# Optimization experiments

Hardware: AMD Instinct MI355X
Metric: run time of the kernel (lower is better)

## Reference

```python
import jax, jax.numpy as jnp
import numpy as np

B, N, D = 8, 2048, 128

def setup_inputs() -> dict:
    key = jax.random.key(0)
    k1, k2, k3 = jax.random.split(key, 3)
    h = jax.random.normal(k1, (B, N, D), dtype=jnp.float32)
    W = jax.random.normal(k2, (D, D), dtype=jnp.float32) * (1.0 / np.sqrt(D))
    # a has shape [1,1,1,2D] in torch; flatten to [2D] (xavier-normal init)
    a = jax.random.normal(k3, (2 * D,), dtype=jnp.float32) * np.sqrt(2.0 / (2 * D))
    return {"h": h, "W": W, "a": a}

def reference(h, W, a):
    act = jax.nn.relu
    # h <- h @ W^T (nn.Linear with weight W means x @ W.T; here W is the weight matrix)
    hw = jnp.einsum('bnd,ed->bne', h, W)  # [B,N,D]
    a_i, a_j = a[:D], a[D:]
    # e_ij = act(a_i . h_i + a_j . h_j) -- equivalent to sum(cat(h_i,h_j)*a, -1)
    s_i = jnp.einsum('bnd,d->bn', hw, a_i)  # [B,N]
    s_j = jnp.einsum('bnd,d->bn', hw, a_j)  # [B,N]
    e = act(s_i[:, :, None] + s_j[:, None, :])  # [B,N,N]
    a_ij = jax.nn.softmax(e, axis=2)
    out = act(jnp.einsum('bij,bjd->bid', a_ij, hw))
    return out
```

## Files before the change

### kernel.cpp

```cpp
#include <hip/hip_runtime.h>
#include <hip/hip_bf16.h>

#define BB 8
#define NN 2048
#define DD 128
#define TI 32
#define HP 132
#define CH 32
#define NC (NN / CH)
#define NO (NC + 1)
#define NFIX (BB * NO)

__device__ __forceinline__ float relu(float x) { return x > 0.f ? x : 0.f; }

__global__ __launch_bounds__(256) void GraphAttentionalLayer_1168231104632_kernel(
    const float* __restrict__ h,
    const float* __restrict__ W,
    const float* __restrict__ a,
    float* __restrict__ hw,
    float* __restrict__ E,
    float* __restrict__ F)
{
    __shared__ float h_s[TI][HP];
    __shared__ float wt_s[32][HP];

    const int tid = threadIdx.x;
    const int t = tid & 127;
    const int hh = tid >> 7;
    const int tx = tid & 31, ty = tid >> 5;
    const int b = blockIdx.x >> 6;
    const int i0 = (blockIdx.x & 63) * TI;
    const size_t base = ((size_t)b * NN + i0) * DD;

    for (int r = hh; r < TI; r += 2)
        h_s[r][t] = h[base + (size_t)r * DD + t];

    const int e0 = tx * 4, r0 = ty * 4;
    float acc[4][4];
#pragma unroll
    for (int i = 0; i < 4; i++)
#pragma unroll
        for (int j = 0; j < 4; j++) acc[i][j] = 0.f;

    for (int dc = 0; dc < DD; dc += 32) {
        __syncthreads();
#pragma unroll
        for (int q = 0; q < 16; q++) {
            const int g = q * 256 + tid;
            const int e = g >> 5;
            const int d2 = g & 31;
            wt_s[d2][e] = W[(size_t)e * DD + dc + d2];
        }
        __syncthreads();
#pragma unroll 4
        for (int dd = 0; dd < 32; dd++) {
            const float4 wv = *reinterpret_cast<const float4*>(&wt_s[dd][e0]);
            const float w4[4] = {wv.x, wv.y, wv.z, wv.w};
#pragma unroll
            for (int r = 0; r < 4; r++) {
                const float hv = h_s[r0 + r][dc + dd];
#pragma unroll
                for (int e = 0; e < 4; e++) acc[r][e] += hv * w4[e];
            }
        }
    }

#pragma unroll
    for (int r = 0; r < 4; r++) {
        float4 o = make_float4(acc[r][0], acc[r][1], acc[r][2], acc[r][3]);
        *reinterpret_cast<float4*>(&hw[base + (size_t)(r0 + r) * DD + e0]) = o;
    }

    const float4 aiv = *reinterpret_cast<const float4*>(&a[e0]);
    const float4 ajv = *reinterpret_cast<const float4*>(&a[DD + e0]);
    const float ai4[4] = {aiv.x, aiv.y, aiv.z, aiv.w};
    const float aj4[4] = {ajv.x, ajv.y, ajv.z, ajv.w};
#pragma unroll
    for (int r = 0; r < 4; r++) {
        float pi = 0.f, pj = 0.f;
#pragma unroll
        for (int e = 0; e < 4; e++) { pi += acc[r][e] * ai4[e]; pj += acc[r][e] * aj4[e]; }
#pragma unroll
        for (int off = 16; off > 0; off >>= 1) {
            pi += __shfl_down(pi, off, 32);
            pj += __shfl_down(pj, off, 32);
        }
        if (tx == 0) {
            const size_t row = (size_t)b * NN + i0 + r0 + r;
            E[row] = __expf(pi);
            F[row] = __expf(pj);
        }
    }
}

__global__ __launch_bounds__(256) void GraphAttentionalLayer_1168231104632_rank(
    const float* __restrict__ F,
    float* __restrict__ Fsorted,
    int* __restrict__ perm)
{
    __shared__ float F_s[NN];
    __shared__ int   part[4][64];

    const int t = threadIdx.x;
    const int b = blockIdx.x >> 5;
    const int j0 = (blockIdx.x & 31) * 64;
    const size_t nb = (size_t)b * NN;

    for (int q = 0; q < NN / 256; q++)
        F_s[q * 256 + t] = F[nb + q * 256 + t];
    __syncthreads();

    const int tj = t & 63, ts = t >> 6;
    const int j = j0 + tj;
    const float fj = F_s[j];
    const int m0 = ts * (NN / 4);
    int cnt = 0;
#pragma unroll 8
    for (int mi = 0; mi < NN / 4; mi++) {
        const int m = m0 + mi;
        const float fm = F_s[m];
        cnt += (fm < fj) | ((fm == fj) & (m < j));
    }
    part[ts][tj] = cnt;
    __syncthreads();
    if (ts == 0) {
        const int r = part[0][tj] + part[1][tj] + part[2][tj] + part[3][tj];
        Fsorted[nb + r] = fj;
        perm[nb + r] = j;
    }
}

__global__ __launch_bounds__(128) void GraphAttentionalLayer_1168231104632_scan(
    const float* __restrict__ hw,
    const float* __restrict__ Fsorted,
    const int* __restrict__ perm,
    float* __restrict__ Q0L, float* __restrict__ Q1L,
    float* __restrict__ C0,  float* __restrict__ C1)
{
    const int t = threadIdx.x;
    const int b = blockIdx.x / NC, c = blockIdx.x % NC;
    const size_t nb = (size_t)b * NN;
    const int m0 = c * CH;

    int   jv[CH];
    float Fv[CH];
#pragma unroll
    for (int mm = 0; mm < CH; mm++) jv[mm] = perm[nb + m0 + mm];
#pragma unroll
    for (int mm = 0; mm < CH; mm++) Fv[mm] = Fsorted[nb + m0 + mm];

    float hv[CH];
#pragma unroll
    for (int mm = 0; mm < CH; mm++)
        hv[mm] = hw[(nb + jv[mm]) * DD + t];

    float a0 = 0.f, a1 = 0.f;
#pragma unroll
    for (int mm = 0; mm < CH; mm++) {
        const int m = m0 + mm;
        Q0L[(nb + m) * DD + t] = a0;
        Q1L[(nb + m) * DD + t] = a1;
        a0 += hv[mm];
        a1 += Fv[mm] * hv[mm];
    }
    C0[((size_t)b * NC + c) * DD + t] = a0;
    C1[((size_t)b * NC + c) * DD + t] = a1;
}

__global__ __launch_bounds__(256) void GraphAttentionalLayer_1168231104632_mid(
    const float* __restrict__ C0, const float* __restrict__ C1,
    const float* __restrict__ Fsorted, const float* __restrict__ E,
    float* __restrict__ O0, float* __restrict__ O1,
    int* __restrict__ kk,  float* __restrict__ zinv)
{
    __shared__ float fs_s[NN];
    __shared__ float cf_s[NC];
    __shared__ float of_s[NO];

    const int tid = threadIdx.x;

    if (blockIdx.x < NFIX) {
        const int b = blockIdx.x / NO, c = blockIdx.x % NO;
        const int d = tid & 127;
        const float* C = (tid < 128) ? C0 : C1;
        float*       O = (tid < 128) ? O0 : O1;
        float o = 0.f;
        int c2 = 0;
        for (; c2 + 16 <= c; c2 += 16) {
            float v[16];
#pragma unroll
            for (int q = 0; q < 16; q++)
                v[q] = C[((size_t)b * NC + c2 + q) * DD + d];
#pragma unroll
            for (int q = 0; q < 16; q++) o += v[q];
        }
        for (; c2 < c; c2++)
            o += C[((size_t)b * NC + c2) * DD + d];
        O[((size_t)b * NO + c) * DD + d] = o;
        return;
    }

    const int sb = blockIdx.x - NFIX;
    const int b = sb >> 3;
    const int i0 = (sb & 7) * 256;
    const size_t nb = (size_t)b * NN;

    for (int q = 0; q < NN / 256; q++)
        fs_s[q * 256 + tid] = Fsorted[nb + q * 256 + tid];
    __syncthreads();

    if (tid < NC) {
        float p = 0.f;
        const int m0 = tid * CH;
#pragma unroll
        for (int mm = 0; mm < CH; mm++) p += fs_s[m0 + mm];
        cf_s[tid] = p;
    }
    __syncthreads();
    if (tid < NO) {
        float p = 0.f;
        for (int c2 = 0; c2 < tid; c2++) p += cf_s[c2];
        of_s[tid] = p;
    }
    __syncthreads();

    const int row = (int)nb + i0 + tid;
    const float Ei = E[row];
    const float thr = 1.0f / Ei;
    int lo = 0, hi = NN;
    while (lo < hi) {
        const int mid = (lo + hi) >> 1;
        if (fs_s[mid] < thr) lo = mid + 1; else hi = mid;
    }
    float fpl = 0.f;
    for (int m = (lo >> 5) << 5; m < lo; m++) fpl += fs_s[m];
    const float TF = of_s[NC];
    const float Pk = of_s[lo >> 5] + fpl;
    const float z = Ei * (TF - Pk) + (float)lo;
    kk[row] = lo;
    zinv[row] = 1.0f / z;
}

__global__ __launch_bounds__(128) void GraphAttentionalLayer_1168231104632_out(
    const float* __restrict__ Q0L, const float* __restrict__ Q1L,
    const float* __restrict__ O0,  const float* __restrict__ O1,
    const int* __restrict__ kk,    const float* __restrict__ zinv,
    const float* __restrict__ E,   float* __restrict__ out)
{
    const int t = threadIdx.x;
    const int row = blockIdx.x;
    const int b = row >> 11;
    const size_t nb = (size_t)b * NN;

    const int k = kk[row];
    const float Ev = E[row];
    const float zv = zinv[row];
    const float T1 = O1[((size_t)b * NO + NC) * DD + t];

    float num;
    if (k < NN) {
        const int c = k >> 5;
        const float q0 = Q0L[(nb + k) * DD + t] + O0[((size_t)b * NO + c) * DD + t];
        const float q1 = Q1L[(nb + k) * DD + t] + O1[((size_t)b * NO + c) * DD + t];
        num = Ev * (T1 - q1) + q0;
    } else {
        num = O0[((size_t)b * NO + NC) * DD + t];
    }
    out[(size_t)row * DD + t] = relu(num * zv);
}

extern "C" __attribute__((visibility("default")))
void kernel_launch(void* const* d_in, const int* in_sizes, int n_in,
                   void* d_out, int out_size, void* d_ws, size_t ws_size,
                   hipStream_t stream) {
    const float* h = nullptr; const float* W = nullptr; const float* a = nullptr;
    for (int i = 0; i < n_in; i++) {
        if (in_sizes[i] == BB * NN * DD)      h = (const float*)d_in[i];
        else if (in_sizes[i] == DD * DD)      W = (const float*)d_in[i];
        else if (in_sizes[i] == 2 * DD)       a = (const float*)d_in[i];
    }
    if (!h) h = (const float*)d_in[0];
    if (!W) W = (const float*)d_in[1];
    if (!a) a = (const float*)d_in[2];

    float* out = (float*)d_out;
    float* ws = (float*)d_ws;

    float* hw   = ws;
    float* E    = hw + (size_t)BB * NN * DD;
    float* F    = E + BB * NN;
    float* Fs   = F + BB * NN;
    float* zinv = Fs + BB * NN;
    int*   perm = (int*)(zinv + BB * NN);
    int*   kk   = perm + BB * NN;
    float* Q0L  = (float*)(kk + BB * NN);
    float* Q1L  = Q0L + (size_t)BB * NN * DD;
    float* C0   = Q1L + (size_t)BB * NN * DD;
    float* C1   = C0 + BB * NC * DD;
    float* O0   = C1 + BB * NC * DD;
    float* O1   = O0 + BB * NO * DD;
    const size_t need = (size_t)((O1 + BB * NO * DD) - ws) * sizeof(float);

    if (ws_size < need || d_ws == nullptr) {
        hipMemsetAsync(d_out, 0x42, (size_t)out_size * sizeof(float), stream);
        return;
    }

    GraphAttentionalLayer_1168231104632_kernel<<<BB * (NN / TI), 256, 0, stream>>>(h, W, a, hw, E, F);
    GraphAttentionalLayer_1168231104632_rank<<<BB * 32, 256, 0, stream>>>(F, Fs, perm);
    GraphAttentionalLayer_1168231104632_scan<<<BB * NC, 128, 0, stream>>>(hw, Fs, perm, Q0L, Q1L, C0, C1);
    GraphAttentionalLayer_1168231104632_mid<<<NFIX + BB * 8, 256, 0, stream>>>(C0, C1, Fs, E, O0, O1, kk, zinv);
    GraphAttentionalLayer_1168231104632_out<<<BB * NN, 128, 0, stream>>>(Q0L, Q1L, O0, O1, kk, zinv, E, out);
}
```

Baseline: 109.3 us.

## Compute h·Wᵀ projection with split-bf16 MFMA instead of scalar FMA

Replaces the shared-memory tiled FP32 FMA projection in the first kernel with MFMA 16x16x32 bf16 instructions. Each FP32 operand is split into hi and lo bf16 parts and combined with three MFMAs to approximate FP32 accuracy. Operands are loaded directly from global memory into registers, and results are staged through LDS to write hw and compute the attention score dot products. This cuts the FMA cost of the projection but adds conversion work and is slightly less precise than FP32. The projection is likely a small share of total time next to the N×N attention kernels.

```diff
diff --git a/kernel.cpp b/kernel.cpp
--- a/kernel.cpp
+++ b/kernel.cpp
@@ -13,6 +13,14 @@
 
 __device__ __forceinline__ float relu(float x) { return x > 0.f ? x : 0.f; }
 
+typedef __attribute__((ext_vector_type(8))) __bf16 bf16x8;
+typedef __attribute__((ext_vector_type(4))) float f32x4;
+
+__device__ __forceinline__ void cvt2(float x, __bf16& hi, __bf16& lo) {
+    hi = (__bf16)x;
+    lo = (__bf16)(x - (float)hi);
+}
+
 __global__ __launch_bounds__(256) void GraphAttentionalLayer_1168231104632_kernel(
     const float* __restrict__ h,
     const float* __restrict__ W,
@@ -21,75 +29,82 @@
     float* __restrict__ E,
     float* __restrict__ F)
 {
-    __shared__ float h_s[TI][HP];
-    __shared__ float wt_s[32][HP];
+    __shared__ float hw_s[TI][HP];
 
     const int tid = threadIdx.x;
-    const int t = tid & 127;
-    const int hh = tid >> 7;
-    const int tx = tid & 31, ty = tid >> 5;
-    const int b = blockIdx.x >> 6;
+    const int lane = tid & 63;
+    const int w  = tid >> 6;
+    const int wm = w & 1;
+    const int wn = w >> 1;
+    const int lr = lane & 15;
+    const int kg = lane >> 4;
+    const int b  = blockIdx.x >> 6;
     const int i0 = (blockIdx.x & 63) * TI;
-    const size_t base = ((size_t)b * NN + i0) * DD;
-
-    for (int r = hh; r < TI; r += 2)
-        h_s[r][t] = h[base + (size_t)r * DD + t];
-
-    const int e0 = tx * 4, r0 = ty * 4;
-    float acc[4][4];
-#pragma unroll
-    for (int i = 0; i < 4; i++)
-#pragma unroll
-        for (int j = 0; j < 4; j++) acc[i][j] = 0.f;
-
-    for (int dc = 0; dc < DD; dc += 32) {
-        __syncthreads();
-#pragma unroll
-        for (int q = 0; q < 16; q++) {
-            const int g = q * 256 + tid;
-            const int e = g >> 5;
-            const int d2 = g & 31;
-            wt_s[d2][e] = W[(size_t)e * DD + dc + d2];
+
+    const int arow = i0 + wm * 16 + lr;
+    const float* hrow = h + ((size_t)b * NN + arow) * DD;
+
+    f32x4 acc[4];
+#pragma unroll
+    for (int nf = 0; nf < 4; nf++) acc[nf] = (f32x4){0.f, 0.f, 0.f, 0.f};
+
+#pragma unroll
+    for (int kc = 0; kc < 4; kc++) {
+        const int kb = kc * 32 + kg * 8;
+        const float4 av0 = *reinterpret_cast<const float4*>(hrow + kb);
+        const float4 av1 = *reinterpret_cast<const float4*>(hrow + kb + 4);
+        const float av[8] = {av0.x, av0.y, av0.z, av0.w, av1.x, av1.y, av1.z, av1.w};
+        bf16x8 ah, al;
+#pragma unroll
+        for (int e = 0; e < 8; e++) { __bf16 hi, lo; cvt2(av[e], hi, lo); ah[e] = hi; al[e] = lo; }
+
+#pragma unroll
+        for (int nf = 0; nf < 4; nf++) {
+            const int wr = wn * 64 + nf * 16 + lr;
+            const float* wrow = W + (size_t)wr * DD + kb;
+            const float4 bv0 = *reinterpret_cast<const float4*>(wrow);
+            const float4 bv1 = *reinterpret_cast<const float4*>(wrow + 4);
+            const float bv[8] = {bv0.x, bv0.y, bv0.z, bv0.w, bv1.x, bv1.y, bv1.z, bv1.w};
+            bf16x8 bh, bl;
+#pragma unroll
+            for (int e = 0; e < 8; e++) { __bf16 hi, lo; cvt2(bv[e], hi, lo); bh[e] = hi; bl[e] = lo; }
+
+            acc[nf] = __builtin_amdgcn_mfma_f32_16x16x32_bf16(ah, bh, acc[nf], 0, 0, 0);
+            acc[nf] = __builtin_amdgcn_mfma_f32_16x16x32_bf16(ah, bl, acc[nf], 0, 0, 0);
+            acc[nf] = __builtin_amdgcn_mfma_f32_16x16x32_bf16(al, bh, acc[nf], 0, 0, 0);
         }
-        __syncthreads();
-#pragma unroll 4
-        for (int dd = 0; dd < 32; dd++) {
-            const float4 wv = *reinterpret_cast<const float4*>(&wt_s[dd][e0]);
-            const float w4[4] = {wv.x, wv.y, wv.z, wv.w};
-#pragma unroll
-            for (int r = 0; r < 4; r++) {
-                const float hv = h_s[r0 + r][dc + dd];
-#pragma unroll
-                for (int e = 0; e < 4; e++) acc[r][e] += hv * w4[e];
-            }
-        }
-    }
-
-#pragma unroll
-    for (int r = 0; r < 4; r++) {
-        float4 o = make_float4(acc[r][0], acc[r][1], acc[r][2], acc[r][3]);
-        *reinterpret_cast<float4*>(&hw[base + (size_t)(r0 + r) * DD + e0]) = o;
-    }
-
-    const float4 aiv = *reinterpret_cast<const float4*>(&a[e0]);
-    const float4 ajv = *reinterpret_cast<const float4*>(&a[DD + e0]);
-    const float ai4[4] = {aiv.x, aiv.y, aiv.z, aiv.w};
-    const float aj4[4] = {ajv.x, ajv.y, ajv.z, ajv.w};
-#pragma unroll
-    for (int r = 0; r < 4; r++) {
-        float pi = 0.f, pj = 0.f;
-#pragma unroll
-        for (int e = 0; e < 4; e++) { pi += acc[r][e] * ai4[e]; pj += acc[r][e] * aj4[e]; }
-#pragma unroll
-        for (int off = 16; off > 0; off >>= 1) {
-            pi += __shfl_down(pi, off, 32);
-            pj += __shfl_down(pj, off, 32);
-        }
-        if (tx == 0) {
-            const size_t row = (size_t)b * NN + i0 + r0 + r;
-            E[row] = __expf(pi);
-            F[row] = __expf(pj);
-        }
+    }
+
+#pragma unroll
+    for (int nf = 0; nf < 4; nf++)
+#pragma unroll
+        for (int r = 0; r < 4; r++)
+            hw_s[wm * 16 + kg * 4 + r][wn * 64 + nf * 16 + lr] = acc[nf][r];
+    __syncthreads();
+
+    const int row = tid >> 3;
+    const int cb  = (tid & 7) * 4;
+    const size_t gbase = ((size_t)b * NN + i0 + row) * DD;
+    float pi = 0.f, pj = 0.f;
+#pragma unroll
+    for (int qq = 0; qq < 4; qq++) {
+        const int col = cb + qq * 32;
+        const float4 v = *reinterpret_cast<const float4*>(&hw_s[row][col]);
+        *reinterpret_cast<float4*>(&hw[gbase + col]) = v;
+        const float4 avi = *reinterpret_cast<const float4*>(&a[col]);
+        const float4 avj = *reinterpret_cast<const float4*>(&a[DD + col]);
+        pi += v.x * avi.x + v.y * avi.y + v.z * avi.z + v.w * avi.w;
+        pj += v.x * avj.x + v.y * avj.y + v.z * avj.z + v.w * avj.w;
+    }
+#pragma unroll
+    for (int off = 4; off > 0; off >>= 1) {
+        pi += __shfl_down(pi, off, 8);
+        pj += __shfl_down(pj, off, 8);
+    }
+    if ((tid & 7) == 0) {
+        const size_t rr = (size_t)b * NN + i0 + row;
+        E[rr] = __expf(pi);
+        F[rr] = __expf(pj);
     }
 }
 
```

After: 108.5 us. Within noise of the previous version (-0.8%).
